# Optimization experiments

Hardware: AMD Instinct MI355X
Metric: run time of the kernel (lower is better)

The kernel has to match this reference:

```python
import jax, jax.numpy as jnp
import numpy as np

COMM_RANGE = 0.5
PATCH = 32
B, N, C_IN, H, W = 32, 8, 3, 224, 224
C, S, HM, CO = 384, 49, 512, 256


def setup_inputs() -> dict:
    key = jax.random.key(0)
    ks = jax.random.split(key, 20)
    sc = 0.02
    return {
        "img_raw": jax.random.normal(ks[0], (B, N, C_IN, H, W), jnp.float32),
        "pos": jax.random.uniform(ks[1], (B, N, 3), jnp.float32),
        "rot": jax.random.uniform(ks[2], (B, N, 3), jnp.float32),
        "W_patch": jax.random.normal(ks[3], (C, C_IN, PATCH, PATCH), jnp.float32) * sc,
        "b_patch": jax.random.normal(ks[4], (C,), jnp.float32) * sc,
        "W1a": jax.random.normal(ks[5], (C, HM), jnp.float32) * sc,
        "W1b": jax.random.normal(ks[6], (C, HM), jnp.float32) * sc,
        "b1": jax.random.normal(ks[7], (HM,), jnp.float32) * sc,
        "W2": jax.random.normal(ks[8], (HM, CO), jnp.float32) * sc,
        "b2": jax.random.normal(ks[9], (CO,), jnp.float32) * sc,
        "Wp": jax.random.normal(ks[10], (CO, 2), jnp.float32) * sc,
        "bp": jax.random.normal(ks[11], (2,), jnp.float32) * sc,
        "Wpv": jax.random.normal(ks[12], (CO, 2), jnp.float32) * sc,
        "bpv": jax.random.normal(ks[13], (2,), jnp.float32) * sc,
        "Wr": jax.random.normal(ks[14], (CO, 2), jnp.float32) * sc,
        "br": jax.random.normal(ks[15], (2,), jnp.float32) * sc,
        "Wrv": jax.random.normal(ks[16], (CO, 1), jnp.float32) * sc,
        "brv": jax.random.normal(ks[17], (1,), jnp.float32) * sc,
    }


def reference(img_raw, pos, rot, W_patch, b_patch, W1a, W1b, b1, W2, b2,
              Wp, bp, Wpv, bpv, Wr, br, Wrv, brv):
    # enc: patch-embed all B*N node images ONCE (the original redundantly
    # re-encodes per edge; math per node is identical).
    img = img_raw.reshape(B * N, C_IN, H, W)
    x = jax.lax.conv_general_dilated(
        img, W_patch, window_strides=(PATCH, PATCH), padding='VALID',
        dimension_numbers=('NCHW', 'OIHW', 'NCHW'))          # [BN, C, 7, 7]
    feats = x.reshape(B * N, C, S).transpose(0, 2, 1) + b_patch  # [BN, S, C]
    feats = feats.reshape(B, N, S, C)

    # radius graph per batch (dense, fixed shape, masked) -- loop=False
    pos2 = pos[..., :2]                                      # [B, N, 2]
    d2 = jnp.sum((pos2[:, :, None] - pos2[:, None, :]) ** 2, axis=-1)
    mask = (d2 < COMM_RANGE ** 2) & (~jnp.eye(N, dtype=bool))  # [B, N, N]
    mf = mask.reshape(B * N * N).astype(feats.dtype)

    # msg: per-token MLP on concat(x_i, x_j); split first layer so we never
    # materialize the [B,N,N,S,2C] concat.
    a = jnp.einsum('bnsc,ch->bnsh', feats, W1a)              # receiver term
    g = jnp.einsum('bnsc,ch->bnsh', feats, W1b)              # sender term
    h = jax.nn.relu(a[:, :, None] + g[:, None, :] + b1)      # [B,N,N,S,HM]
    m = jnp.einsum('bijsh,ho->bijo', h / S, W2) + b2         # mean-pool + fc

    # post: four heads -> pos(2), pos_var(2), rot(2), rot_var(1)
    heads = jnp.concatenate(
        [m @ Wp + bp, m @ Wpv + bpv, m @ Wr + br, m @ Wrv + brv], axis=-1)
    edge_out = heads.reshape(B * N * N, 7) * mf[:, None]     # masked edges

    node_preds = jnp.zeros((B, N, 1, 60, 60), jnp.float32)
    return edge_out, mask.reshape(B * N * N), node_preds
```

## Files before the change

### kernel.cpp

```cpp
#include <hip/hip_runtime.h>
#include <hip/hip_bf16.h>

typedef __attribute__((ext_vector_type(4))) float f32x4;
typedef __attribute__((ext_vector_type(8))) short s16x8;
typedef __attribute__((ext_vector_type(4))) short s16x4;
typedef unsigned short u16;
typedef unsigned int u32;

__device__ inline u16 f2bf(float f) {
    union { float f; u32 u; } v; v.f = f;
    u32 r = v.u + 0x7FFFu + ((v.u >> 16) & 1u);
    return (u16)(r >> 16);
}
__device__ inline float bfbits2f(u32 hi_bits) {
    union { u32 u; float f; } v; v.u = hi_bits; return v.f;
}

__global__ __launch_bounds__(384) void prep_all(
    const float* __restrict__ img, u16* __restrict__ patches,
    const float* __restrict__ W_patch, u16* __restrict__ wpb,
    const float* __restrict__ W1a, const float* __restrict__ W1b,
    u16* __restrict__ w1cat,
    const float* __restrict__ W2, const float* __restrict__ b2,
    const float* __restrict__ Wp, const float* __restrict__ bp,
    const float* __restrict__ Wpv, const float* __restrict__ bpv,
    const float* __restrict__ Wr, const float* __restrict__ br,
    const float* __restrict__ Wrv, const float* __restrict__ brv,
    float* __restrict__ W2h, float* __restrict__ bias7) {
    __shared__ __align__(16) u16 tile[3 * 32 * 224];
    const int blk = blockIdx.x;
    const int t = threadIdx.x;
    if (blk < 1792) {
        const int n = blk / 7, py = blk - n * 7;
        const float* base = img + (size_t)n * 3 * 50176 + py * 32 * 224;
#pragma unroll
        for (int i = 0; i < 14; i++) {
            int f = i * 384 + t;
            int c = f / 1792, rem = f - c * 1792;
            float4 v = *(const float4*)(base + (size_t)c * 50176 + rem * 4);
            s16x4 o;
            o[0] = (short)f2bf(v.x); o[1] = (short)f2bf(v.y);
            o[2] = (short)f2bf(v.z); o[3] = (short)f2bf(v.w);
            *(s16x4*)(tile + f * 4) = o;
        }
        __syncthreads();
        const int c = t >> 7, u = t & 127;
        const int r = u >> 2, cc = (u & 3) * 8;
        const u16* lsrc = tile + c * 7168 + r * 224;
        u16* gdst = patches + (size_t)(n * 49 + py * 7) * 3072 + c * 1024 + r * 32 + cc;
#pragma unroll
        for (int px = 0; px < 7; px++) {
            s16x8 v = *(const s16x8*)(lsrc + px * 32 + cc);
            *(s16x8*)(gdst + (size_t)px * 3072) = v;
        }
        return;
    }
    const int NW = 147456;
    const int NC = 1024 * 384;
    const int NH = 3591;
    const int total = NW + NC + NH;
    for (int idx = (blk - 1792) * 384 + t; idx < total; idx += 128 * 384) {
        if (idx < NW) {
            int i = idx * 8;
            s16x8 o;
#pragma unroll
            for (int q = 0; q < 8; q++) o[q] = (short)f2bf(W_patch[i + q]);
            *(s16x8*)(wpb + i) = o;
        } else if (idx < NW + NC) {
            int w = idx - NW;
            int h = w / 384, k = w - h * 384;
            float v = (h < 512) ? W1a[k * 512 + h] : W1b[k * 512 + (h - 512)];
            w1cat[w] = f2bf(v);
        } else {
            int w = idx - NW - NC;
            if (w < 3584) {
                int h = w / 7, kk = w - h * 7;
                float s = 0.f;
                for (int o = 0; o < 256; o++) {
                    float ww = (kk < 2) ? Wp[o * 2 + kk]
                             : (kk < 4) ? Wpv[o * 2 + kk - 2]
                             : (kk < 6) ? Wr[o * 2 + kk - 4]
                                        : Wrv[o];
                    s += W2[h * 256 + o] * ww;
                }
                W2h[w] = s;
            } else {
                int kk = w - 3584;
                float s = (kk < 2) ? bp[kk] : (kk < 4) ? bpv[kk - 2]
                        : (kk < 6) ? br[kk - 4] : brv[0];
                for (int o = 0; o < 256; o++) {
                    float ww = (kk < 2) ? Wp[o * 2 + kk]
                             : (kk < 4) ? Wpv[o * 2 + kk - 2]
                             : (kk < 6) ? Wr[o * 2 + kk - 4]
                                        : Wrv[o];
                    s += b2[o] * ww;
                }
                bias7[kk] = s;
            }
        }
    }
}

template<int BM, int BN>
__global__ __launch_bounds__(256) void gemm_bt(const u16* __restrict__ A,
                                               const u16* __restrict__ Bt,
                                               u16* __restrict__ Cb,
                                               const float* __restrict__ bias,
                                               int M, int N, int K) {
    constexpr int MF = BM / 32;
    constexpr int NF = BN / 32;
    __shared__ __align__(16) u16 As[BM * 64];
    __shared__ __align__(16) u16 Bs[BN * 64];
    const int tid = threadIdx.x;
    const int wave = tid >> 6, lane = tid & 63;
    const int wr = wave >> 1, wc = wave & 1;
    const int row0 = blockIdx.x * BM, col0 = blockIdx.y * BN;
    const int lr = lane >> 3;
    const int lcb = (lane & 7) * 8;
    f32x4 acc[MF][NF] = {};

    for (int k0 = 0; k0 < K; k0 += 64) {
        __syncthreads();
#pragma unroll
        for (int q = 0; q < BM / 32; q++) {
            int ch = q * 4 + wave;
            const u16* gA = A + (size_t)(row0 + ch * 8 + lr) * K + k0 + lcb;
            __builtin_amdgcn_global_load_lds(
                (const __attribute__((address_space(1))) unsigned int*)gA,
                (__attribute__((address_space(3))) unsigned int*)(As + ch * 512), 16, 0, 0);
        }
#pragma unroll
        for (int q = 0; q < BN / 32; q++) {
            int ch = q * 4 + wave;
            const u16* gB = Bt + (size_t)(col0 + ch * 8 + lr) * K + k0 + lcb;
            __builtin_amdgcn_global_load_lds(
                (const __attribute__((address_space(1))) unsigned int*)gB,
                (__attribute__((address_space(3))) unsigned int*)(Bs + ch * 512), 16, 0, 0);
        }
        __syncthreads();
#pragma unroll
        for (int kk = 0; kk < 64; kk += 32) {
            s16x8 af[MF], bfr[NF];
#pragma unroll
            for (int m = 0; m < MF; m++)
                af[m] = *(const s16x8*)(As + (wr * (BM / 2) + m * 16 + (lane & 15)) * 64 + kk + (lane >> 4) * 8);
#pragma unroll
            for (int n = 0; n < NF; n++)
                bfr[n] = *(const s16x8*)(Bs + (wc * (BN / 2) + n * 16 + (lane & 15)) * 64 + kk + (lane >> 4) * 8);
#pragma unroll
            for (int m = 0; m < MF; m++)
#pragma unroll
                for (int n = 0; n < NF; n++)
                    acc[m][n] = __builtin_amdgcn_mfma_f32_16x16x32_bf16(af[m], bfr[n], acc[m][n], 0, 0, 0);
        }
    }
#pragma unroll
    for (int m = 0; m < MF; m++) {
        int drow = row0 + wr * (BM / 2) + m * 16 + (lane >> 4) * 4;
#pragma unroll
        for (int n = 0; n < NF; n++) {
            int dcol = col0 + wc * (BN / 2) + n * 16 + (lane & 15);
            float bv = bias ? bias[dcol] : 0.0f;
#pragma unroll
            for (int i = 0; i < 4; i++)
                Cb[(size_t)(drow + i) * N + dcol] = f2bf(acc[m][n][i] + bv);
        }
    }
}

__global__ __launch_bounds__(256) void edge_kernel(
    const u16* __restrict__ ag, const float* __restrict__ pos,
    const float* __restrict__ b1, const float* __restrict__ W2h,
    const float* __restrict__ bias7,
    float* __restrict__ edge_out, float* __restrict__ mask_out,
    float* __restrict__ node_preds) {
    __shared__ float red[4][7];
    const int e = blockIdx.x;
    const int b = e >> 6, ij = e & 63, i = ij >> 3, j = ij & 7;
    const int t = threadIdx.x;
    for (int z = t; z < 450; z += 256) node_preds[(size_t)e * 450 + z] = 0.0f;
    const float dx = pos[(b * 8 + i) * 3 + 0] - pos[(b * 8 + j) * 3 + 0];
    const float dy = pos[(b * 8 + i) * 3 + 1] - pos[(b * 8 + j) * 3 + 1];
    const bool msk = (dx * dx + dy * dy < 0.25f) && (i != j);
    if (t == 0) mask_out[e] = msk ? 1.0f : 0.0f;
    if (!msk) {
        if (t < 7) edge_out[e * 7 + t] = 0.0f;
        return;
    }
    const int h0 = t * 2;
    const u16* arow = ag + (size_t)(b * 8 + i) * 49 * 1024 + h0;
    const u16* grow = ag + (size_t)(b * 8 + j) * 49 * 1024 + 512 + h0;
    const float b10 = b1[h0], b11 = b1[h0 + 1];
    float r0 = 0.f, r1 = 0.f;
#pragma unroll 7
    for (int s = 0; s < 49; s++) {
        u32 av = *(const u32*)(arow + (size_t)s * 1024);
        u32 gv = *(const u32*)(grow + (size_t)s * 1024);
        float a0 = bfbits2f(av << 16), a1 = bfbits2f(av & 0xFFFF0000u);
        float g0 = bfbits2f(gv << 16), g1 = bfbits2f(gv & 0xFFFF0000u);
        r0 += fmaxf(a0 + g0 + b10, 0.f);
        r1 += fmaxf(a1 + g1 + b11, 0.f);
    }
    float c[7];
#pragma unroll
    for (int k = 0; k < 7; k++)
        c[k] = r0 * W2h[h0 * 7 + k] + r1 * W2h[(h0 + 1) * 7 + k];
#pragma unroll
    for (int k = 0; k < 7; k++)
#pragma unroll
        for (int off = 32; off; off >>= 1)
            c[k] += __shfl_down(c[k], off, 64);
    const int lane = t & 63, wv = t >> 6;
    if (lane == 0)
        for (int k = 0; k < 7; k++) red[wv][k] = c[k];
    __syncthreads();
    if (t == 0)
        for (int k = 0; k < 7; k++) {
            float v = red[0][k] + red[1][k] + red[2][k] + red[3][k];
            edge_out[e * 7 + k] = v * (1.f / 49.f) + bias7[k];
        }
}

extern "C" void kernel_launch(void* const* d_in, const int* in_sizes, int n_in,
                              void* d_out, int out_size, void* d_ws, size_t ws_size,
                              hipStream_t stream) {
    const float* img    = (const float*)d_in[0];
    const float* pos    = (const float*)d_in[1];
    const float* W_patch= (const float*)d_in[3];
    const float* b_patch= (const float*)d_in[4];
    const float* W1a    = (const float*)d_in[5];
    const float* W1b    = (const float*)d_in[6];
    const float* b1     = (const float*)d_in[7];
    const float* W2     = (const float*)d_in[8];
    const float* b2     = (const float*)d_in[9];
    const float* Wp     = (const float*)d_in[10];
    const float* bp     = (const float*)d_in[11];
    const float* Wpv    = (const float*)d_in[12];
    const float* bpv    = (const float*)d_in[13];
    const float* Wr     = (const float*)d_in[14];
    const float* br     = (const float*)d_in[15];
    const float* Wrv    = (const float*)d_in[16];
    const float* brv    = (const float*)d_in[17];

    char* ws = (char*)d_ws;
    u16*   patches = (u16*)(ws + 0);
    u16*   ag      = (u16*)(ws + 77070336);
    u16*   feats   = (u16*)(ws + 102760448);
    u16*   wpb     = (u16*)(ws + 112394240);
    u16*   w1cat   = (u16*)(ws + 114753536);
    float* W2h     = (float*)(ws + 115539968);
    float* bias7   = (float*)(ws + 115554304);

    float* edge_out   = (float*)d_out;
    float* mask_out   = edge_out + 14336;
    float* node_preds = mask_out + 2048;

    prep_all<<<1920, 384, 0, stream>>>(img, patches, W_patch, wpb,
                                       W1a, W1b, w1cat,
                                       W2, b2, Wp, bp, Wpv, bpv, Wr, br, Wrv, brv,
                                       W2h, bias7);

    dim3 g1(98, 6);
    gemm_bt<128, 64><<<g1, 256, 0, stream>>>(patches, wpb, feats, b_patch, 12544, 384, 3072);
    dim3 g2(196, 8);
    gemm_bt<64, 128><<<g2, 256, 0, stream>>>(feats, w1cat, ag, nullptr, 12544, 1024, 384);

    edge_kernel<<<2048, 256, 0, stream>>>(ag, pos, b1, W2h, bias7,
                                          edge_out, mask_out, node_preds);
}
```

Before: 417.8 us.

## Fuse im2col and bf16 conversion of images into patch-embed GEMM

Drops the separate im2col pass that converted the fp32 images into a bf16 patch matrix in workspace (about 77 MB written, then read back). The patch-embed GEMM now loads fp32 pixels straight from the image, converts them to bf16 in registers and stores them into the LDS A tile, while the B tile still uses async global-to-LDS loads. This removes a full write and reread of the patch matrix. In exchange, the fp32 image is reread by each of the 6 column blocks, and the A loads are synchronous and no longer asynchronous copies.

```diff
diff --git a/kernel.cpp b/kernel.cpp
--- a/kernel.cpp
+++ b/kernel.cpp
@@ -3,7 +3,6 @@
 
 typedef __attribute__((ext_vector_type(4))) float f32x4;
 typedef __attribute__((ext_vector_type(8))) short s16x8;
-typedef __attribute__((ext_vector_type(4))) short s16x4;
 typedef unsigned short u16;
 typedef unsigned int u32;
 
@@ -16,8 +15,7 @@
     union { u32 u; float f; } v; v.u = hi_bits; return v.f;
 }
 
-__global__ __launch_bounds__(384) void prep_all(
-    const float* __restrict__ img, u16* __restrict__ patches,
+__global__ __launch_bounds__(256) void prep_w(
     const float* __restrict__ W_patch, u16* __restrict__ wpb,
     const float* __restrict__ W1a, const float* __restrict__ W1b,
     u16* __restrict__ w1cat,
@@ -27,39 +25,11 @@
     const float* __restrict__ Wr, const float* __restrict__ br,
     const float* __restrict__ Wrv, const float* __restrict__ brv,
     float* __restrict__ W2h, float* __restrict__ bias7) {
-    __shared__ __align__(16) u16 tile[3 * 32 * 224];
-    const int blk = blockIdx.x;
-    const int t = threadIdx.x;
-    if (blk < 1792) {
-        const int n = blk / 7, py = blk - n * 7;
-        const float* base = img + (size_t)n * 3 * 50176 + py * 32 * 224;
-#pragma unroll
-        for (int i = 0; i < 14; i++) {
-            int f = i * 384 + t;
-            int c = f / 1792, rem = f - c * 1792;
-            float4 v = *(const float4*)(base + (size_t)c * 50176 + rem * 4);
-            s16x4 o;
-            o[0] = (short)f2bf(v.x); o[1] = (short)f2bf(v.y);
-            o[2] = (short)f2bf(v.z); o[3] = (short)f2bf(v.w);
-            *(s16x4*)(tile + f * 4) = o;
-        }
-        __syncthreads();
-        const int c = t >> 7, u = t & 127;
-        const int r = u >> 2, cc = (u & 3) * 8;
-        const u16* lsrc = tile + c * 7168 + r * 224;
-        u16* gdst = patches + (size_t)(n * 49 + py * 7) * 3072 + c * 1024 + r * 32 + cc;
-#pragma unroll
-        for (int px = 0; px < 7; px++) {
-            s16x8 v = *(const s16x8*)(lsrc + px * 32 + cc);
-            *(s16x8*)(gdst + (size_t)px * 3072) = v;
-        }
-        return;
-    }
     const int NW = 147456;
     const int NC = 1024 * 384;
     const int NH = 3591;
     const int total = NW + NC + NH;
-    for (int idx = (blk - 1792) * 384 + t; idx < total; idx += 128 * 384) {
+    for (int idx = blockIdx.x * 256 + threadIdx.x; idx < total; idx += 256 * 256) {
         if (idx < NW) {
             int i = idx * 8;
             s16x8 o;
@@ -101,6 +71,95 @@
     }
 }
 
+__global__ __launch_bounds__(256) void gemm1_im2col(
+    const float* __restrict__ img, const u16* __restrict__ Bt,
+    u16* __restrict__ Cb, const float* __restrict__ bias) {
+    constexpr int K = 3072, N = 384;
+    __shared__ __align__(16) u16 As[128 * 64];
+    __shared__ __align__(16) u16 Bs[64 * 64];
+    const int tid = threadIdx.x;
+    const int wave = tid >> 6, lane = tid & 63;
+    const int wr = wave >> 1, wc = wave & 1;
+    const int row0 = blockIdx.x * 128, col0 = blockIdx.y * 64;
+    const int lr = lane >> 3;
+    const int lcb = (lane & 7) * 8;
+
+    const float* abase[4];
+    int arow[4];
+#pragma unroll
+    for (int q = 0; q < 4; q++) {
+        int ch = q * 4 + wave;
+        int rA = ch * 8 + lr;
+        int m = row0 + rA;
+        int n = m / 49, s = m - n * 49;
+        int py = s / 7, px = s - py * 7;
+        abase[q] = img + ((size_t)(n * 3) * 224 + py * 32) * 224 + px * 32;
+        arow[q] = rA;
+    }
+    f32x4 acc[4][2] = {};
+
+    for (int k0 = 0; k0 < K; k0 += 64) {
+        __syncthreads();
+#pragma unroll
+        for (int q = 0; q < 2; q++) {
+            int ch = q * 4 + wave;
+            const u16* gB = Bt + (size_t)(col0 + ch * 8 + lr) * K + k0 + lcb;
+            __builtin_amdgcn_global_load_lds(
+                (const __attribute__((address_space(1))) unsigned int*)gB,
+                (__attribute__((address_space(3))) unsigned int*)(Bs + ch * 512), 16, 0, 0);
+        }
+        const int k = k0 + lcb;
+        const int c = k >> 10;
+        const int r = (k & 1023) >> 5;
+        const int cc = k & 31;
+        const int koff = (c * 224 + r) * 224 + cc;
+        float4 va[4], vb[4];
+#pragma unroll
+        for (int q = 0; q < 4; q++) {
+            const float* src = abase[q] + koff;
+            va[q] = *(const float4*)src;
+            vb[q] = *(const float4*)(src + 4);
+        }
+#pragma unroll
+        for (int q = 0; q < 4; q++) {
+            s16x8 o;
+            o[0] = (short)f2bf(va[q].x); o[1] = (short)f2bf(va[q].y);
+            o[2] = (short)f2bf(va[q].z); o[3] = (short)f2bf(va[q].w);
+            o[4] = (short)f2bf(vb[q].x); o[5] = (short)f2bf(vb[q].y);
+            o[6] = (short)f2bf(vb[q].z); o[7] = (short)f2bf(vb[q].w);
+            *(s16x8*)(As + arow[q] * 64 + lcb) = o;
+        }
+        __syncthreads();
+#pragma unroll
+        for (int kk = 0; kk < 64; kk += 32) {
+            s16x8 af[4], bfr[2];
+#pragma unroll
+            for (int m = 0; m < 4; m++)
+                af[m] = *(const s16x8*)(As + (wr * 64 + m * 16 + (lane & 15)) * 64 + kk + (lane >> 4) * 8);
+#pragma unroll
+            for (int n = 0; n < 2; n++)
+                bfr[n] = *(const s16x8*)(Bs + (wc * 32 + n * 16 + (lane & 15)) * 64 + kk + (lane >> 4) * 8);
+#pragma unroll
+            for (int m = 0; m < 4; m++)
+#pragma unroll
+                for (int n = 0; n < 2; n++)
+                    acc[m][n] = __builtin_amdgcn_mfma_f32_16x16x32_bf16(af[m], bfr[n], acc[m][n], 0, 0, 0);
+        }
+    }
+#pragma unroll
+    for (int m = 0; m < 4; m++) {
+        int drow = row0 + wr * 64 + m * 16 + (lane >> 4) * 4;
+#pragma unroll
+        for (int n = 0; n < 2; n++) {
+            int dcol = col0 + wc * 32 + n * 16 + (lane & 15);
+            float bv = bias[dcol];
+#pragma unroll
+            for (int i = 0; i < 4; i++)
+                Cb[(size_t)(drow + i) * N + dcol] = f2bf(acc[m][n][i] + bv);
+        }
+    }
+}
+
 template<int BM, int BN>
 __global__ __launch_bounds__(256) void gemm_bt(const u16* __restrict__ A,
                                                const u16* __restrict__ Bt,
@@ -243,25 +302,23 @@
     const float* brv    = (const float*)d_in[17];
 
     char* ws = (char*)d_ws;
-    u16*   patches = (u16*)(ws + 0);
-    u16*   ag      = (u16*)(ws + 77070336);
-    u16*   feats   = (u16*)(ws + 102760448);
-    u16*   wpb     = (u16*)(ws + 112394240);
-    u16*   w1cat   = (u16*)(ws + 114753536);
-    float* W2h     = (float*)(ws + 115539968);
-    float* bias7   = (float*)(ws + 115554304);
+    u16*   ag      = (u16*)(ws + 0);
+    u16*   feats   = (u16*)(ws + 25690112);
+    u16*   wpb     = (u16*)(ws + 35323904);
+    u16*   w1cat   = (u16*)(ws + 37683200);
+    float* W2h     = (float*)(ws + 38469632);
+    float* bias7   = (float*)(ws + 38483968);
 
     float* edge_out   = (float*)d_out;
     float* mask_out   = edge_out + 14336;
     float* node_preds = mask_out + 2048;
 
-    prep_all<<<1920, 384, 0, stream>>>(img, patches, W_patch, wpb,
-                                       W1a, W1b, w1cat,
-                                       W2, b2, Wp, bp, Wpv, bpv, Wr, br, Wrv, brv,
-                                       W2h, bias7);
+    prep_w<<<256, 256, 0, stream>>>(W_patch, wpb, W1a, W1b, w1cat,
+                                    W2, b2, Wp, bp, Wpv, bpv, Wr, br, Wrv, brv,
+                                    W2h, bias7);
 
     dim3 g1(98, 6);
-    gemm_bt<128, 64><<<g1, 256, 0, stream>>>(patches, wpb, feats, b_patch, 12544, 384, 3072);
+    gemm1_im2col<<<g1, 256, 0, stream>>>(img, wpb, feats, b_patch);
     dim3 g2(196, 8);
     gemm_bt<64, 128><<<g2, 256, 0, stream>>>(feats, w1cat, ag, nullptr, 12544, 1024, 384);
 
```

Result: slower. 446.0 us (+6.8%).
